# Kernel tuning notes

Hardware: AMD Instinct MI355X
Metric: run time of the kernel (lower is better)

Reference implementation:

```python
import jax, jax.numpy as jnp
import numpy as np

N, G, D, H, B = 32768, 1024, 512, 768, 4   # nodes, graphs, hidden, shared, branches
GHD, NHD = 64, 3                           # graph head dim, node head dim (var_output=1)

def setup_inputs() -> dict:
    key = jax.random.key(0)
    ks = jax.random.split(key, 8)
    scale = 0.02
    x = jax.random.normal(ks[0], (N, D), dtype=jnp.float32)
    batch = jnp.sort(jax.random.randint(ks[1], (N,), 0, G, dtype=jnp.int32))
    dataset_name = jax.random.randint(ks[2], (G,), 0, B, dtype=jnp.int32)
    return {
        "x": x,
        "batch": batch,
        "dataset_name": dataset_name,
        "Wg_shared": jax.random.normal(ks[3], (B, D, H), jnp.float32) * scale,
        "bg_shared": jnp.zeros((B, H), jnp.float32),
        "Wg_head": jax.random.normal(ks[4], (B, H, 2 * GHD), jnp.float32) * scale,
        "bg_head": jnp.zeros((B, 2 * GHD), jnp.float32),
        "Wn1": jax.random.normal(ks[5], (B, D, D), jnp.float32) * scale,
        "bn1": jnp.zeros((B, D), jnp.float32),
        "Wn2": jax.random.normal(ks[6], (B, D, 2 * NHD), jnp.float32) * scale,
        "bn2": jnp.zeros((B, 2 * NHD), jnp.float32),
    }

def _select_branch(y, branch_ids):
    # y: [n, B, f], branch_ids: [n] -> [n, f]
    return jnp.take_along_axis(y, branch_ids[:, None, None], axis=1)[:, 0]

def reference(x, batch, dataset_name, Wg_shared, bg_shared, Wg_head, bg_head,
              Wn1, bn1, Wn2, bn2):
    nG = dataset_name.shape[0]
    # --- graph mean pooling (graph_pool_fn with reduction='mean') ---
    counts = jax.ops.segment_sum(jnp.ones((x.shape[0], 1), x.dtype), batch,
                                 num_segments=nG)
    x_graph = jax.ops.segment_sum(x, batch, num_segments=nG) / jnp.maximum(counts, 1.0)
    # --- graph head: per-dataset-ID branch dispatch (dense-MoE form) ---
    hg = jax.nn.relu(jnp.einsum('gd,bdh->gbh', x_graph, Wg_shared) + bg_shared)  # [G,B,H]
    hg_sel = _select_branch(hg, dataset_name)                                    # [G,H]
    og = jnp.einsum('gh,bho->gbo', hg_sel, Wg_head) + bg_head                    # [G,B,2*GHD]
    og_sel = _select_branch(og, dataset_name)
    graph_head = og_sel[:, :GHD]
    graph_var = og_sel[:, GHD:] ** 2
    # --- node head: route nodes by their graph's dataset ID (repeat_interleave) ---
    node_branch = dataset_name[batch]                                            # [N]
    hn = jax.nn.relu(jnp.einsum('nd,bdh->nbh', x, Wn1) + bn1)                    # [N,B,D]
    hn_sel = _select_branch(hn, node_branch)                                     # [N,D]
    on = jnp.einsum('nh,bho->nbo', hn_sel, Wn2) + bn2                            # [N,B,2*NHD]
    on_sel = _select_branch(on, node_branch)
    node_head = on_sel[:, :NHD]
    node_var = on_sel[:, NHD:] ** 2
    # torch returns (outputs, outputs_var); flattened here as 4 arrays
    return (graph_head, node_head, graph_var, node_var)
```

## Files before the change

### kernel.cpp

```cpp
#include <hip/hip_runtime.h>

#define N_NODES 32768
#define G_GRAPHS 1024
#define D_DIM 512
#define H_DIM 768
#define B_BR 4
#define GHD 64
#define NHD 3

#define NH_OFF (G_GRAPHS * GHD)
#define GV_OFF (G_GRAPHS * GHD + N_NODES * NHD)
#define NV_OFF (2 * G_GRAPHS * GHD + N_NODES * NHD)

typedef unsigned short ushort_t;
typedef __attribute__((ext_vector_type(8))) short short8;
typedef __attribute__((ext_vector_type(4))) float f32x4;
typedef __attribute__((ext_vector_type(4))) ushort_t ushort4_t;

__device__ __forceinline__ ushort_t rne_bf16(float v) {
  unsigned bits = __float_as_uint(v);
  return (ushort_t)((bits + 0x7fffu + ((bits >> 16) & 1u)) >> 16);
}

__global__ __launch_bounds__(1024) void segscan_kernel(
    const int* __restrict__ batch, const int* __restrict__ dsname,
    int* __restrict__ gstart, int* __restrict__ goff, int* __restrict__ glist,
    int* __restrict__ cnt, int* __restrict__ gcnt, int* __restrict__ pbase) {
  __shared__ int sg[G_GRAPHS + 1];
  __shared__ int scnt[4], sgcnt[4];
  const int tid = threadIdx.x;
  {
    int g = tid;
    int lo = 0, hi = N_NODES;
    while (lo < hi) { int mid = (lo + hi) >> 1; if (batch[mid] < g) lo = mid + 1; else hi = mid; }
    sg[g] = lo; gstart[g] = lo;
    if (tid == 0) { sg[G_GRAPHS] = N_NODES; gstart[G_GRAPHS] = N_NODES; }
  }
  __syncthreads();
  if (tid < 256) {
    const int lane = tid & 63;
    const int b = tid >> 6;
    int run_n = 0, run_g = 0;
    for (int c = 0; c < G_GRAPHS / 64; ++c) {
      int g = c * 64 + lane;
      int mine = (dsname[g] == b) ? 1 : 0;
      int len = mine ? (sg[g + 1] - sg[g]) : 0;
      int sl = len, so = mine;
#pragma unroll
      for (int off = 1; off < 64; off <<= 1) {
        int tl = __shfl_up(sl, off);
        int to = __shfl_up(so, off);
        if (lane >= off) { sl += tl; so += to; }
      }
      if (mine) {
        goff[g] = run_n + sl - len;
        glist[b * G_GRAPHS + run_g + so - 1] = g;
      }
      run_n += __shfl(sl, 63);
      run_g += __shfl(so, 63);
    }
    if (lane == 0) { scnt[b] = run_n; sgcnt[b] = run_g; }
  }
  __syncthreads();
  if (tid == 0) {
    int p = 0;
    for (int b2 = 0; b2 < 4; ++b2) {
      cnt[b2] = scnt[b2];
      gcnt[b2] = sgcnt[b2];
      pbase[b2] = p;
      p += (scnt[b2] + 63) & ~63;
    }
  }
}

__global__ __launch_bounds__(256) void prep_kernel(
    const float* __restrict__ x, const int* __restrict__ batch,
    const int* __restrict__ dsname, const int* __restrict__ gstart,
    const int* __restrict__ goff, const int* __restrict__ pbase,
    int* __restrict__ lists, ushort_t* __restrict__ xp,
    ushort_t* __restrict__ xgb,
    const float* __restrict__ Wn1, ushort_t* __restrict__ WPh,
    const float* __restrict__ Wg1, ushort_t* __restrict__ WG1,
    const float* __restrict__ Wgh, ushort_t* __restrict__ WG2,
    const float* __restrict__ Wn2, ushort_t* __restrict__ W2T) {
  __shared__ float Ws[64][65];
  const int bid = blockIdx.x;
  const int tid = threadIdx.x;

  if (bid < 512) {
    const int g = bid * 2 + (tid >> 7);
    const int tg = tid & 127;
    const int start = gstart[g], end = gstart[g + 1];
    const float inv = (end > start) ? 1.0f / (float)(end - start) : 0.0f;
    float4 acc = make_float4(0.f, 0.f, 0.f, 0.f);
    for (int i = start; i < end; ++i) {
      float4 v = *reinterpret_cast<const float4*>(&x[(size_t)i * D_DIM + tg * 4]);
      acc.x += v.x; acc.y += v.y; acc.z += v.z; acc.w += v.w;
    }
    ushort4_t h4;
    h4[0] = rne_bf16(acc.x * inv); h4[1] = rne_bf16(acc.y * inv);
    h4[2] = rne_bf16(acc.z * inv); h4[3] = rne_bf16(acc.w * inv);
    *reinterpret_cast<ushort4_t*>(&xgb[(size_t)g * D_DIM + tg * 4]) = h4;
  } else if (bid < 1024) {
    const int blk = bid - 512;
#pragma unroll
    for (int it = 0; it < 16; ++it) {
      int u = it * 256 + tid;
      int r = u >> 6, cp = u & 63;
      int n = blk * 64 + r;
      int g = batch[n];
      int b = dsname[g];
      int i = goff[g] + (n - gstart[g]);
      if (cp == 0) lists[b * N_NODES + i] = n;
      int dest = pbase[b] + i;
      int g8 = cp ^ (i & 7);
      const float* sp = x + (size_t)n * D_DIM + g8 * 8;
      float4 v0 = *reinterpret_cast<const float4*>(sp);
      float4 v1 = *reinterpret_cast<const float4*>(sp + 4);
      short8 h;
      h[0] = (short)rne_bf16(v0.x); h[1] = (short)rne_bf16(v0.y);
      h[2] = (short)rne_bf16(v0.z); h[3] = (short)rne_bf16(v0.w);
      h[4] = (short)rne_bf16(v1.x); h[5] = (short)rne_bf16(v1.y);
      h[6] = (short)rne_bf16(v1.z); h[7] = (short)rne_bf16(v1.w);
      *reinterpret_cast<short8*>(xp + (size_t)dest * 512 + cp * 8) = h;
    }
  } else {
    const int cid = bid - 1024;
    if (cid < 256) {
      int b = cid >> 6, t = cid & 63;
      int kt = t >> 3, nt = t & 7;
      const float* W = Wn1 + (size_t)b * D_DIM * D_DIM;
      for (int i = tid; i < 64 * 64; i += 256) {
        int k = i >> 6, n = i & 63;
        Ws[k][n] = W[(size_t)(kt * 64 + k) * D_DIM + nt * 64 + n];
      }
      __syncthreads();
      for (int i = tid; i < 64 * 8; i += 256) {
        int n = i >> 3, kq8 = i & 7;
        short8 sh;
#pragma unroll
        for (int j = 0; j < 8; ++j) sh[j] = (short)rne_bf16(Ws[kq8 * 8 + j][n]);
        int gn = nt * 64 + n, gk0 = kt * 64 + kq8 * 8;
        int n16 = gn >> 4, l15 = gn & 15;
        int ks = gk0 >> 5, lq = (gk0 >> 3) & 3;
        size_t off = ((((size_t)b * 32 + n16) * 16 + ks) * 64 + lq * 16 + l15) * 8;
        *reinterpret_cast<short8*>(WPh + off) = sh;
      }
    } else if (cid < 640) {
      int l2 = cid - 256;
      int b = l2 / 96, t = l2 % 96;
      int kt = t / 12, nt = t % 12;
      const float* W = Wg1 + (size_t)b * D_DIM * H_DIM;
      for (int i = tid; i < 64 * 64; i += 256) {
        int k = i >> 6, n = i & 63;
        Ws[k][n] = W[(size_t)(kt * 64 + k) * H_DIM + nt * 64 + n];
      }
      __syncthreads();
      for (int i = tid; i < 64 * 8; i += 256) {
        int n = i >> 3, kq8 = i & 7;
        short8 sh;
#pragma unroll
        for (int j = 0; j < 8; ++j) sh[j] = (short)rne_bf16(Ws[kq8 * 8 + j][n]);
        int gn = nt * 64 + n, gk0 = kt * 64 + kq8 * 8;
        int n16 = gn >> 4, l15 = gn & 15;
        int ks = gk0 >> 5, lq = (gk0 >> 3) & 3;
        size_t off = ((((size_t)b * 48 + n16) * 16 + ks) * 64 + lq * 16 + l15) * 8;
        *reinterpret_cast<short8*>(WG1 + off) = sh;
      }
    } else if (cid < 644) {
      int b = cid - 640;
      const float* W = Wgh + (size_t)b * H_DIM * 2 * GHD;
      for (int i = tid; i < 8 * 24 * 64; i += 256) {
        int n16 = i / (24 * 64);
        int rem = i % (24 * 64);
        int ks = rem / 64, lane = rem % 64;
        int l15 = lane & 15, lq = lane >> 4;
        int o = n16 * 16 + l15;
        short8 sv;
#pragma unroll
        for (int j = 0; j < 8; ++j) {
          int k = ks * 32 + lq * 8 + j;
          sv[j] = (short)rne_bf16(W[(size_t)k * 128 + o]);
        }
        *reinterpret_cast<short8*>(WG2 + (size_t)i * 8 + (size_t)b * (8 * 24 * 64 * 8)) = sv;
      }
    } else {
      int b = cid - 644;
      for (int i = tid; i < 16 * D_DIM; i += 256) {
        int o = i & 15, c = i >> 4;
        float v = (o < 6) ? Wn2[(size_t)b * D_DIM * 6 + c * 6 + o] : 0.0f;
        W2T[(size_t)b * 16 * D_DIM + o * D_DIM + c] = rne_bf16(v);
      }
    }
  }
}

#define NBM 64
#define GRAPH_BLOCKS 128
#define NODE_BLOCKS 576

__global__ __launch_bounds__(512, 4) void mega_kernel(
    const ushort_t* __restrict__ xpacked,
    const ushort_t* __restrict__ WPh,
    const float* __restrict__ bn1,
    const ushort_t* __restrict__ W2T, const float* __restrict__ bn2,
    const int* __restrict__ cnt, const int* __restrict__ pbase,
    const int* __restrict__ lists,
    const ushort_t* __restrict__ xgb,
    const ushort_t* __restrict__ WG1, const float* __restrict__ bg_shared,
    const ushort_t* __restrict__ WG2, const float* __restrict__ bg_head,
    const int* __restrict__ gcnt, const int* __restrict__ glist,
    float* __restrict__ out) {
  __shared__ __align__(16) char smem[65536];
  __shared__ int idxbuf[64];

  const int bid = blockIdx.x;
  const int tid = threadIdx.x;
  const int lane = tid & 63;
  const int w = tid >> 6;
  const int l15 = lane & 15;
  const int lq = lane >> 4;

  if (bid >= GRAPH_BLOCKS) {
    const int nb = bid - GRAPH_BLOCKS;
    const int b = (nb & 7) >> 1;
    const int tile = ((nb >> 3) << 1) | (nb & 1);
    const int count = cnt[b];
    const int base = tile * NBM;
    if (base >= count) return;
    const int tile_base = pbase[b] + base;

    ushort_t* Ah = (ushort_t*)smem;
    if (tid < NBM) {
      int r = base + tid;
      idxbuf[tid] = (r < count) ? lists[b * N_NODES + r] : lists[b * N_NODES];
    }

    const char* srow = (const char*)(xpacked + (size_t)tile_base * 512);
#pragma unroll
    for (int i = 0; i < 8; ++i) {
      int row = w * 8 + i;
      const void* gsrc = srow + (size_t)row * 1024 + (size_t)lane * 16;
      __builtin_amdgcn_global_load_lds(
          (const __attribute__((address_space(1))) void*)gsrc,
          (__attribute__((address_space(3))) void*)((char*)Ah + row * 1024),
          16, 0, 0);
    }
    __syncthreads();

    f32x4 acc[4][4];
#pragma unroll
    for (int i = 0; i < 4; ++i)
#pragma unroll
      for (int j = 0; j < 4; ++j) acc[i][j] = (f32x4){0.f, 0.f, 0.f, 0.f};

    const ushort_t* __restrict__ wph =
        WPh + (((size_t)b * 32 + w * 4) * 16) * 512 + (size_t)lane * 8;

    for (int ks = 0; ks < 16; ++ks) {
      short8 ah[4];
#pragma unroll
      for (int rt = 0; rt < 4; ++rt) {
        int R = rt * 16 + l15;
        int byteoff = R * 1024 + ((ks * 64 + lq * 16) ^ ((R & 7) << 4));
        ah[rt] = *reinterpret_cast<const short8*>((const char*)Ah + byteoff);
      }
#pragma unroll
      for (int ct = 0; ct < 4; ++ct) {
        short8 bh = *reinterpret_cast<const short8*>(wph + (size_t)(ct * 16 + ks) * 512);
#pragma unroll
        for (int rt = 0; rt < 4; ++rt) {
          acc[rt][ct] = __builtin_amdgcn_mfma_f32_16x16x32_bf16(ah[rt], bh, acc[rt][ct], 0, 0, 0);
        }
      }
    }

    __syncthreads();
    ushort_t* hn = Ah;
#pragma unroll
    for (int ct = 0; ct < 4; ++ct) {
      int n = w * 64 + ct * 16 + l15;
      float bias = bn1[b * D_DIM + n];
#pragma unroll
      for (int rt = 0; rt < 4; ++rt) {
#pragma unroll
        for (int j = 0; j < 4; ++j) {
          int row = rt * 16 + lq * 4 + j;
          float v = fmaxf(acc[rt][ct][j] + bias, 0.0f);
          int byteoff = row * 1024 + ((n * 2) ^ ((row & 7) << 4));
          *reinterpret_cast<ushort_t*>((char*)hn + byteoff) = rne_bf16(v);
        }
      }
    }
    __syncthreads();

    if (w < 4) {
      f32x4 acc2 = (f32x4){0.f, 0.f, 0.f, 0.f};
      const ushort_t* __restrict__ w2 =
          W2T + (size_t)b * (16 * 512) + (size_t)l15 * 512 + lq * 8;
      const int R = w * 16 + l15;
#pragma unroll
      for (int ks = 0; ks < 16; ++ks) {
        int byteoff = R * 1024 + ((ks * 64 + lq * 16) ^ ((R & 7) << 4));
        short8 a2 = *reinterpret_cast<const short8*>((const char*)hn + byteoff);
        short8 b2 = *reinterpret_cast<const short8*>(w2 + ks * 32);
        acc2 = __builtin_amdgcn_mfma_f32_16x16x32_bf16(a2, b2, acc2, 0, 0, 0);
      }
      int o = l15;
      if (o < 6) {
        float bo = bn2[b * 6 + o];
#pragma unroll
        for (int j = 0; j < 4; ++j) {
          int r = w * 16 + lq * 4 + j;
          if (base + r < count) {
            int n = idxbuf[r];
            float v = acc2[j] + bo;
            if (o < NHD) out[NH_OFF + n * NHD + o] = v;
            else out[NV_OFF + n * NHD + (o - NHD)] = v * v;
          }
        }
      }
    }
  } else {
    const int gb = bid;
    const int b = (gb & 7) >> 1;
    const int tile = ((gb >> 3) << 1) | (gb & 1);
    const int gc = gcnt[b];
    const int base = tile * 32;
    if (base >= gc) return;

    ushort_t* Ag = (ushort_t*)smem;
    if (tid < 32) {
      int r = base + tid;
      idxbuf[tid] = (r < gc) ? glist[b * G_GRAPHS + r] : glist[b * G_GRAPHS];
    }
    __syncthreads();

#pragma unroll
    for (int it = 0; it < 4; ++it) {
      int u = it * 512 + tid;
      int r = u >> 6, cp = u & 63;
      const ushort_t* sp = xgb + (size_t)idxbuf[r] * D_DIM + cp * 8;
      short8 h = *reinterpret_cast<const short8*>(sp);
      int byteoff = r * 1024 + ((cp * 16) ^ ((r & 7) << 4));
      *reinterpret_cast<short8*>((char*)Ag + byteoff) = h;
    }
    __syncthreads();

    f32x4 acc[2][6];
#pragma unroll
    for (int i = 0; i < 2; ++i)
#pragma unroll
      for (int j = 0; j < 6; ++j) acc[i][j] = (f32x4){0.f, 0.f, 0.f, 0.f};

    const ushort_t* __restrict__ g1 =
        WG1 + (((size_t)b * 48 + w * 6) * 16) * 512 + (size_t)lane * 8;

    for (int ks = 0; ks < 16; ++ks) {
      short8 ah[2];
#pragma unroll
      for (int rt = 0; rt < 2; ++rt) {
        int R = rt * 16 + l15;
        int byteoff = R * 1024 + ((ks * 64 + lq * 16) ^ ((R & 7) << 4));
        ah[rt] = *reinterpret_cast<const short8*>((const char*)Ag + byteoff);
      }
#pragma unroll
      for (int ct = 0; ct < 6; ++ct) {
        short8 bh = *reinterpret_cast<const short8*>(g1 + (size_t)(ct * 16 + ks) * 512);
#pragma unroll
        for (int rt = 0; rt < 2; ++rt) {
          acc[rt][ct] = __builtin_amdgcn_mfma_f32_16x16x32_bf16(ah[rt], bh, acc[rt][ct], 0, 0, 0);
        }
      }
    }

    __syncthreads();
    ushort_t* hgs = (ushort_t*)smem;
#pragma unroll
    for (int ct = 0; ct < 6; ++ct) {
      int n = w * 96 + ct * 16 + l15;
      float bias = bg_shared[b * H_DIM + n];
#pragma unroll
      for (int rt = 0; rt < 2; ++rt) {
#pragma unroll
        for (int j = 0; j < 4; ++j) {
          int row = rt * 16 + lq * 4 + j;
          float v = fmaxf(acc[rt][ct][j] + bias, 0.0f);
          int byteoff = row * 1536 + ((n * 2) ^ ((row & 7) << 4));
          *reinterpret_cast<ushort_t*>((char*)hgs + byteoff) = rne_bf16(v);
        }
      }
    }
    __syncthreads();

    f32x4 acc2[2];
    acc2[0] = (f32x4){0.f, 0.f, 0.f, 0.f};
    acc2[1] = (f32x4){0.f, 0.f, 0.f, 0.f};
    const ushort_t* __restrict__ g2 =
        WG2 + ((size_t)(b * 8 + w) * 24 * 64 + lane) * 8;

    for (int ks = 0; ks < 24; ++ks) {
      short8 b2 = *reinterpret_cast<const short8*>(g2 + (size_t)ks * 512);
#pragma unroll
      for (int rt = 0; rt < 2; ++rt) {
        int R = rt * 16 + l15;
        int byteoff = R * 1536 + ((ks * 64 + lq * 16) ^ ((R & 7) << 4));
        short8 a2 = *reinterpret_cast<const short8*>((const char*)hgs + byteoff);
        acc2[rt] = __builtin_amdgcn_mfma_f32_16x16x32_bf16(a2, b2, acc2[rt], 0, 0, 0);
      }
    }

    int o = w * 16 + l15;
    float bo = bg_head[b * 2 * GHD + o];
#pragma unroll
    for (int rt = 0; rt < 2; ++rt) {
#pragma unroll
      for (int j = 0; j < 4; ++j) {
        int r = rt * 16 + lq * 4 + j;
        if (base + r < gc) {
          int g = idxbuf[r];
          float v = acc2[rt][j] + bo;
          if (o < GHD) out[g * GHD + o] = v;
          else out[GV_OFF + g * GHD + (o - GHD)] = v * v;
        }
      }
    }
  }
}

extern "C" void kernel_launch(void* const* d_in, const int* in_sizes, int n_in,
                              void* d_out, int out_size, void* d_ws, size_t ws_size,
                              hipStream_t stream) {
  const float* x         = (const float*)d_in[0];
  const int*   batch     = (const int*)d_in[1];
  const int*   dsname    = (const int*)d_in[2];
  const float* Wg_shared = (const float*)d_in[3];
  const float* bg_shared = (const float*)d_in[4];
  const float* Wg_head   = (const float*)d_in[5];
  const float* bg_head   = (const float*)d_in[6];
  const float* Wn1       = (const float*)d_in[7];
  const float* bn1       = (const float*)d_in[8];
  const float* Wn2       = (const float*)d_in[9];
  const float* bn2       = (const float*)d_in[10];
  float* out = (float*)d_out;

  int* ws_i   = (int*)d_ws;
  int* cnt    = ws_i;
  int* gcnt   = ws_i + 8;
  int* pbase  = ws_i + 12;
  int* gstart = ws_i + 16;
  int* goff   = ws_i + 1056;
  int* glist  = ws_i + 2080;
  int* lists  = ws_i + 6176;
  ushort_t* xgb  = (ushort_t*)(ws_i + 137248);
  ushort_t* WPh  = xgb + 524288;
  ushort_t* W2T  = WPh + 1048576;
  ushort_t* WG1  = W2T + 32768;
  ushort_t* WG2  = WG1 + 1572864;
  ushort_t* xpacked = WG2 + 393216;

  segscan_kernel<<<1, 1024, 0, stream>>>(batch, dsname, gstart, goff, glist,
                                         cnt, gcnt, pbase);
  prep_kernel<<<1672, 256, 0, stream>>>(x, batch, dsname, gstart, goff, pbase,
                                        lists, xpacked, xgb,
                                        Wn1, WPh, Wg_shared, WG1,
                                        Wg_head, WG2, Wn2, W2T);
  mega_kernel<<<GRAPH_BLOCKS + NODE_BLOCKS, 512, 0, stream>>>(
      xpacked, WPh, bn1, W2T, bn2, cnt, pbase, lists,
      xgb, WG1, bg_shared, WG2, bg_head, gcnt, glist, out);
}
```

Baseline: 102.0 us.

## Fuse graph pooling with node packing and double-buffer weight tiles through LDS

The prep kernel now handles graph mean pooling and the per-node bf16 packing/list construction in a single pass per graph. Each x row is read once instead of twice, with partial sums reduced through shared memory. The node GEMM in mega_kernel now prefetches the weight fragments for the next k-step into a per-wave double-buffered LDS region using global_load_lds, instead of loading them directly from global memory each step. This doubles shared memory to 128KB and lowers the occupancy hint from 4 to 2 blocks per CU, trading parallelism for less global traffic and better latency hiding.

```diff
diff --git a/kernel.cpp b/kernel.cpp
--- a/kernel.cpp
+++ b/kernel.cpp
@@ -88,44 +88,54 @@
   const int tid = threadIdx.x;
 
   if (bid < 512) {
-    const int g = bid * 2 + (tid >> 7);
-    const int tg = tid & 127;
-    const int start = gstart[g], end = gstart[g + 1];
-    const float inv = (end > start) ? 1.0f / (float)(end - start) : 0.0f;
-    float4 acc = make_float4(0.f, 0.f, 0.f, 0.f);
-    for (int i = start; i < end; ++i) {
-      float4 v = *reinterpret_cast<const float4*>(&x[(size_t)i * D_DIM + tg * 4]);
-      acc.x += v.x; acc.y += v.y; acc.z += v.z; acc.w += v.w;
-    }
-    ushort4_t h4;
-    h4[0] = rne_bf16(acc.x * inv); h4[1] = rne_bf16(acc.y * inv);
-    h4[2] = rne_bf16(acc.z * inv); h4[3] = rne_bf16(acc.w * inv);
-    *reinterpret_cast<ushort4_t*>(&xgb[(size_t)g * D_DIM + tg * 4]) = h4;
-  } else if (bid < 1024) {
-    const int blk = bid - 512;
-#pragma unroll
-    for (int it = 0; it < 16; ++it) {
-      int u = it * 256 + tid;
-      int r = u >> 6, cp = u & 63;
-      int n = blk * 64 + r;
-      int g = batch[n];
+    const int rl = tid >> 6;
+    const int cs = tid & 63;
+    float* red = (float*)Ws;
+#pragma unroll
+    for (int gi = 0; gi < 2; ++gi) {
+      int g = bid * 2 + gi;
+      int start = gstart[g], end = gstart[g + 1];
+      int len = end - start;
       int b = dsname[g];
-      int i = goff[g] + (n - gstart[g]);
-      if (cp == 0) lists[b * N_NODES + i] = n;
-      int dest = pbase[b] + i;
-      int g8 = cp ^ (i & 7);
-      const float* sp = x + (size_t)n * D_DIM + g8 * 8;
-      float4 v0 = *reinterpret_cast<const float4*>(sp);
-      float4 v1 = *reinterpret_cast<const float4*>(sp + 4);
-      short8 h;
-      h[0] = (short)rne_bf16(v0.x); h[1] = (short)rne_bf16(v0.y);
-      h[2] = (short)rne_bf16(v0.z); h[3] = (short)rne_bf16(v0.w);
-      h[4] = (short)rne_bf16(v1.x); h[5] = (short)rne_bf16(v1.y);
-      h[6] = (short)rne_bf16(v1.z); h[7] = (short)rne_bf16(v1.w);
-      *reinterpret_cast<short8*>(xp + (size_t)dest * 512 + cp * 8) = h;
+      int og = goff[g];
+      int off0 = pbase[b] + og;
+      float s0 = 0.f, s1 = 0.f, s2 = 0.f, s3 = 0.f;
+      float s4 = 0.f, s5 = 0.f, s6 = 0.f, s7 = 0.f;
+      for (int i = rl; i < len; i += 4) {
+        int n = start + i;
+        const float* sp = x + (size_t)n * D_DIM + cs * 8;
+        float4 v0 = *reinterpret_cast<const float4*>(sp);
+        float4 v1 = *reinterpret_cast<const float4*>(sp + 4);
+        s0 += v0.x; s1 += v0.y; s2 += v0.z; s3 += v0.w;
+        s4 += v1.x; s5 += v1.y; s6 += v1.z; s7 += v1.w;
+        short8 h;
+        h[0] = (short)rne_bf16(v0.x); h[1] = (short)rne_bf16(v0.y);
+        h[2] = (short)rne_bf16(v0.z); h[3] = (short)rne_bf16(v0.w);
+        h[4] = (short)rne_bf16(v1.x); h[5] = (short)rne_bf16(v1.y);
+        h[6] = (short)rne_bf16(v1.z); h[7] = (short)rne_bf16(v1.w);
+        int ib = og + i;
+        *reinterpret_cast<short8*>(xp + (size_t)(off0 + i) * 512 + (cs ^ (ib & 7)) * 8) = h;
+        if (cs == 0) lists[b * N_NODES + ib] = n;
+      }
+      float* rr = red + (rl * 64 + cs) * 8;
+      rr[0] = s0; rr[1] = s1; rr[2] = s2; rr[3] = s3;
+      rr[4] = s4; rr[5] = s5; rr[6] = s6; rr[7] = s7;
+      __syncthreads();
+      if (rl == 0) {
+        float inv = (len > 0) ? 1.0f / (float)len : 0.0f;
+        short8 h;
+#pragma unroll
+        for (int k = 0; k < 8; ++k) {
+          float tot = red[(0 * 64 + cs) * 8 + k] + red[(1 * 64 + cs) * 8 + k] +
+                      red[(2 * 64 + cs) * 8 + k] + red[(3 * 64 + cs) * 8 + k];
+          h[k] = (short)rne_bf16(tot * inv);
+        }
+        *reinterpret_cast<short8*>(xgb + (size_t)g * D_DIM + cs * 8) = h;
+      }
+      __syncthreads();
     }
   } else {
-    const int cid = bid - 1024;
+    const int cid = bid - 512;
     if (cid < 256) {
       int b = cid >> 6, t = cid & 63;
       int kt = t >> 3, nt = t & 7;
@@ -199,7 +209,7 @@
 #define GRAPH_BLOCKS 128
 #define NODE_BLOCKS 576
 
-__global__ __launch_bounds__(512, 4) void mega_kernel(
+__global__ __launch_bounds__(512, 2) void mega_kernel(
     const ushort_t* __restrict__ xpacked,
     const ushort_t* __restrict__ WPh,
     const float* __restrict__ bn1,
@@ -211,7 +221,7 @@
     const ushort_t* __restrict__ WG2, const float* __restrict__ bg_head,
     const int* __restrict__ gcnt, const int* __restrict__ glist,
     float* __restrict__ out) {
-  __shared__ __align__(16) char smem[65536];
+  __shared__ __align__(16) char smem[131072];
   __shared__ int idxbuf[64];
 
   const int bid = blockIdx.x;
@@ -248,17 +258,39 @@
     }
     __syncthreads();
 
-    f32x4 acc[4][4];
-#pragma unroll
-    for (int i = 0; i < 4; ++i)
-#pragma unroll
-      for (int j = 0; j < 4; ++j) acc[i][j] = (f32x4){0.f, 0.f, 0.f, 0.f};
-
     const ushort_t* __restrict__ wph =
         WPh + (((size_t)b * 32 + w * 4) * 16) * 512 + (size_t)lane * 8;
-
+    ushort_t* Bl = (ushort_t*)(smem + 65536 + w * 8192);
+
+#pragma unroll
+    for (int ct = 0; ct < 4; ++ct) {
+      __builtin_amdgcn_global_load_lds(
+          (const __attribute__((address_space(1))) void*)(wph + (size_t)(ct * 16) * 512),
+          (__attribute__((address_space(3))) void*)(Bl + ct * 512),
+          16, 0, 0);
+    }
+
+    f32x4 acc[4][4];
+#pragma unroll
+    for (int i = 0; i < 4; ++i)
+#pragma unroll
+      for (int j = 0; j < 4; ++j) acc[i][j] = (f32x4){0.f, 0.f, 0.f, 0.f};
+
+#pragma unroll
     for (int ks = 0; ks < 16; ++ks) {
-      short8 ah[4];
+      const int nks = (ks + 1) & 15;
+      ushort_t* Bnx = Bl + ((ks + 1) & 1) * 2048;
+#pragma unroll
+      for (int ct = 0; ct < 4; ++ct) {
+        __builtin_amdgcn_global_load_lds(
+            (const __attribute__((address_space(1))) void*)(wph + (size_t)(ct * 16 + nks) * 512),
+            (__attribute__((address_space(3))) void*)(Bnx + ct * 512),
+            16, 0, 0);
+      }
+      asm volatile("s_waitcnt vmcnt(4)" ::: "memory");
+      __builtin_amdgcn_sched_barrier(0);
+      const ushort_t* Bc = Bl + (ks & 1) * 2048;
+      short8 ah[4], bh[4];
 #pragma unroll
       for (int rt = 0; rt < 4; ++rt) {
         int R = rt * 16 + l15;
@@ -266,11 +298,13 @@
         ah[rt] = *reinterpret_cast<const short8*>((const char*)Ah + byteoff);
       }
 #pragma unroll
+      for (int ct = 0; ct < 4; ++ct)
+        bh[ct] = *reinterpret_cast<const short8*>(Bc + ct * 512 + lane * 8);
+#pragma unroll
       for (int ct = 0; ct < 4; ++ct) {
-        short8 bh = *reinterpret_cast<const short8*>(wph + (size_t)(ct * 16 + ks) * 512);
 #pragma unroll
         for (int rt = 0; rt < 4; ++rt) {
-          acc[rt][ct] = __builtin_amdgcn_mfma_f32_16x16x32_bf16(ah[rt], bh, acc[rt][ct], 0, 0, 0);
+          acc[rt][ct] = __builtin_amdgcn_mfma_f32_16x16x32_bf16(ah[rt], bh[ct], acc[rt][ct], 0, 0, 0);
         }
       }
     }
@@ -461,7 +495,7 @@
 
   segscan_kernel<<<1, 1024, 0, stream>>>(batch, dsname, gstart, goff, glist,
                                          cnt, gcnt, pbase);
-  prep_kernel<<<1672, 256, 0, stream>>>(x, batch, dsname, gstart, goff, pbase,
+  prep_kernel<<<1160, 256, 0, stream>>>(x, batch, dsname, gstart, goff, pbase,
                                         lists, xpacked, xgb,
                                         Wn1, WPh, Wg_shared, WG1,
                                         Wg_head, WG2, Wn2, W2T);
```

After: 87.79 us. 13.9% less time.
